# Kernel optimization log

Measured on AMD Instinct MI355X. Metric: run time of the kernel, lower is better.

The kernel has to match this reference:

```python
import jax, jax.numpy as jnp
import numpy as np

NUM_TABLES = 10
EMB_DIM = 3
VOCAB = 1_000_000
N_IDX = 4_000_000
N_BAGS = 100_000


def setup_inputs() -> dict:
    key = jax.random.key(0)
    k_idx, k_off, k_w = jax.random.split(key, 3)
    eb_input = jax.random.randint(k_idx, (N_IDX,), 0, VOCAB, dtype=jnp.int64)
    # EmbeddingBag offsets: sorted, first element must be 0, values in [0, N_IDX)
    eb_offset = jnp.sort(jax.random.randint(k_off, (N_BAGS,), 0, N_IDX, dtype=jnp.int64))
    eb_offset = eb_offset.at[0].set(0)
    # torch.nn.EmbeddingBag default init: N(0, 1)
    W = jax.random.normal(k_w, (NUM_TABLES, VOCAB, EMB_DIM), dtype=jnp.float32)
    return {"eb_input": eb_input, "eb_offset": eb_offset, "W": W}


def _bag_sums(eb_input, eb_offset, W):
    # segment id for each index position: bag b covers [offset[b], offset[b+1])
    n = eb_input.shape[0]
    seg = jnp.searchsorted(eb_offset, jnp.arange(n), side="right") - 1  # [N]
    gathered = W[:, eb_input, :]  # [T, N, D] irregular gather
    # sum-pool per bag for every table
    per_bag = jax.vmap(lambda g: jax.ops.segment_sum(g, seg, num_segments=eb_offset.shape[0]))(gathered)  # [T, B, D]
    return per_bag


def reference(eb_input, eb_offset, W):
    per_bag = _bag_sums(eb_input, eb_offset, W)  # [10, B, 3]
    outs = [per_bag[i] for i in range(NUM_TABLES)]
    outs[5] = jnp.sum(outs[5], axis=1, keepdims=True)  # [B, 1]
    outs[6] = jnp.sum(outs[6], axis=1, keepdims=True)  # [B, 1]
    cat = jnp.concatenate(outs, axis=1)  # [B, 26]
    return jnp.sum(cat, axis=0)  # [26]
```

## Files before the change

### kernel.cpp

```cpp
#include <hip/hip_runtime.h>

#define VOCAB 1000000
#define NUM_TABLES 10
#define OUT_SIZE 26
#define BUCKET_BITS 12
#define BPB 4096
#define NBUCKETS 245
#define CHUNK 4096
#define MAXSRC 1024
#define GSTRIDE 256
#define NPB NBUCKETS
#define NSERIES 30


__global__ void __launch_bounds__(256) scatter_kernel(
    const int* __restrict__ idx, int n,
    unsigned short* __restrict__ scat,
    unsigned int* __restrict__ gs32)
{
    __shared__ unsigned int lcount[256];
    __shared__ unsigned int sc[256];
    __shared__ __align__(16) unsigned short stage[CHUNK];
    const int tid = threadIdx.x;
    lcount[tid] = 0u;
    __syncthreads();

    const int4* idx4 = (const int4*)idx;
    const int n4 = n >> 2;
    const int base4 = blockIdx.x * (CHUNK / 4);
    int4 q[4];
    bool val[4];
    unsigned rank[16];
    unsigned bkt[16];
#pragma unroll
    for (int j = 0; j < 4; ++j) {
        int i4 = base4 + j * 256 + tid;
        val[j] = (i4 < n4);
        if (val[j]) q[j] = idx4[i4];
    }
#pragma unroll
    for (int j = 0; j < 4; ++j) {
        if (val[j]) {
            unsigned v[4] = {(unsigned)q[j].x, (unsigned)q[j].y, (unsigned)q[j].z, (unsigned)q[j].w};
#pragma unroll
            for (int e = 0; e < 4; ++e) {
                bkt[j * 4 + e] = v[e] >> BUCKET_BITS;
                rank[j * 4 + e] = atomicAdd(&lcount[bkt[j * 4 + e]], 1u);
            }
        }
    }
    unsigned trank[3], tbkt[3];
    int tcnt = 0;
    if (blockIdx.x == gridDim.x - 1 && tid == 0) {
        for (int i = n4 * 4; i < n; ++i) {
            unsigned u = (unsigned)idx[i];
            tbkt[tcnt] = u >> BUCKET_BITS;
            trank[tcnt] = atomicAdd(&lcount[tbkt[tcnt]], 1u);
            ++tcnt;
        }
    }
    __syncthreads();
    unsigned cnt = (tid < NBUCKETS) ? lcount[tid] : 0u;
    sc[tid] = cnt;
    __syncthreads();
#pragma unroll
    for (int off = 1; off < 256; off <<= 1) {
        unsigned v = sc[tid];
        unsigned a = (tid >= off) ? sc[tid - off] : 0u;
        __syncthreads();
        sc[tid] = v + a;
        __syncthreads();
    }
    unsigned excl = sc[tid] - cnt;
    if (tid < NBUCKETS) gs32[(size_t)blockIdx.x * GSTRIDE + tid] = excl | (cnt << 16);
    lcount[tid] = excl;
    __syncthreads();
#pragma unroll
    for (int j = 0; j < 4; ++j) {
        if (val[j]) {
            unsigned v[4] = {(unsigned)q[j].x, (unsigned)q[j].y, (unsigned)q[j].z, (unsigned)q[j].w};
#pragma unroll
            for (int e = 0; e < 4; ++e) {
                unsigned k = j * 4 + e;
                stage[lcount[bkt[k]] + rank[k]] = (unsigned short)(v[e] & (BPB - 1));
            }
        }
    }
    if (blockIdx.x == gridDim.x - 1 && tid == 0) {
        for (int i = 0; i < tcnt; ++i) {
            unsigned u = (unsigned)idx[n4 * 4 + i];
            stage[lcount[tbkt[i]] + trank[i]] = (unsigned short)(u & (BPB - 1));
        }
    }
    __syncthreads();
    uint4* dst = (uint4*)(scat + (size_t)blockIdx.x * CHUNK);
    const uint4* src = (const uint4*)stage;
#pragma unroll
    for (int j = 0; j < 2; ++j) dst[j * 256 + tid] = src[j * 256 + tid];
}

__device__ inline float wave_reduce(float v) {
#pragma unroll
    for (int o = 32; o > 0; o >>= 1) v += __shfl_down(v, o, 64);
    return v;
}

__global__ void __launch_bounds__(1024) bucket_reduce_kernel(
    const unsigned short* __restrict__ scat,
    const unsigned int* __restrict__ gs32, int nsrc,
    const float* __restrict__ W,
    float* __restrict__ partials)
{
    __shared__ __align__(16) unsigned int h[BPB];
    __shared__ float sm[16][NSERIES];
    const int b = blockIdx.x;
    const int tid = threadIdx.x;
    for (int i = tid; i < BPB; i += 1024) h[i] = 0u;
    __syncthreads();
    if (tid < nsrc) {
        unsigned g32 = gs32[(size_t)tid * GSTRIDE + b];
        unsigned s = g32 & 0xffffu, c = g32 >> 16;
        const unsigned short* p = scat + (size_t)tid * CHUNK + s;
        unsigned k = 0;
        for (; k + 4 <= c; k += 4) {
            unsigned short a0 = p[k], a1 = p[k + 1], a2 = p[k + 2], a3 = p[k + 3];
            atomicAdd(&h[a0], 1u);
            atomicAdd(&h[a1], 1u);
            atomicAdd(&h[a2], 1u);
            atomicAdd(&h[a3], 1u);
        }
        for (; k < c; ++k) atomicAdd(&h[p[k]], 1u);
    }
    __syncthreads();

    const int nbg = min(BPB, VOCAB - b * BPB) >> 2;
    float acc[NUM_TABLES][3];
#pragma unroll
    for (int t = 0; t < NUM_TABLES; ++t) {
        acc[t][0] = 0.f; acc[t][1] = 0.f; acc[t][2] = 0.f;
    }
    if (tid < nbg) {
        uint4 c4 = ((const uint4*)h)[tid];
        float c0 = (float)c4.x, c1 = (float)c4.y, c2 = (float)c4.z, c3 = (float)c4.w;
        const int g = b * (BPB / 4) + tid;
#pragma unroll
        for (int t = 0; t < NUM_TABLES; ++t) {
            const float4* __restrict__ W4 = (const float4*)(W + (size_t)t * VOCAB * 3);
            float4 w0 = W4[3 * g + 0];
            float4 w1 = W4[3 * g + 1];
            float4 w2 = W4[3 * g + 2];
            acc[t][0] += c0 * w0.x + c1 * w0.w + c2 * w1.z + c3 * w2.y;
            acc[t][1] += c0 * w0.y + c1 * w1.x + c2 * w1.w + c3 * w2.z;
            acc[t][2] += c0 * w0.z + c1 * w1.y + c2 * w2.x + c3 * w2.w;
        }
    }
    const int wave = tid >> 6, lane = tid & 63;
#pragma unroll
    for (int t = 0; t < NUM_TABLES; ++t) {
#pragma unroll
        for (int d = 0; d < 3; ++d) {
            float v = wave_reduce(acc[t][d]);
            if (lane == 0) sm[wave][t * 3 + d] = v;
        }
    }
    __syncthreads();
    if (tid < NSERIES) {
        float v = 0.f;
#pragma unroll
        for (int w = 0; w < 16; ++w) v += sm[w][tid];
        partials[(size_t)tid * NPB + b] = v;
    }
}

__global__ void __launch_bounds__(1024) final_kernel(const float* __restrict__ partials,
                                                     float* __restrict__ out) {
    __shared__ float ts[32];
    const int tid = threadIdx.x;
    const int srs = tid >> 5;
    const int j = tid & 31;
    float v = 0.f;
    if (srs < NSERIES) {
        const float* p = partials + (size_t)srs * NPB;
#pragma unroll
        for (int k = 0; k < 8; ++k) {
            int i = k * 32 + j;
            if (i < NPB) v += p[i];
        }
    }
#pragma unroll
    for (int off = 16; off > 0; off >>= 1) v += __shfl_down(v, off);
    if (j == 0 && srs < NSERIES) ts[srs] = v;
    __syncthreads();
    if (tid < OUT_SIZE) {
        float r;
        if (tid < 15) r = ts[tid];
        else if (tid == 15) r = ts[15] + ts[16] + ts[17];
        else if (tid == 16) r = ts[18] + ts[19] + ts[20];
        else r = ts[tid + 4];
        out[tid] = r;
    }
}


__global__ void zero_kernel_fb(unsigned int* __restrict__ hist, float* __restrict__ out) {
    int i = blockIdx.x * blockDim.x + threadIdx.x;
    int n4 = VOCAB / 4;
    if (i < n4) ((uint4*)hist)[i] = make_uint4(0u, 0u, 0u, 0u);
    if (i < OUT_SIZE) out[i] = 0.0f;
}

__global__ void hist_kernel_fb(const int* __restrict__ idx, unsigned int* __restrict__ hist, int n) {
    int i = blockIdx.x * blockDim.x + threadIdx.x;
    int i4 = i * 4;
    if (i4 + 3 < n) {
        int4 v = ((const int4*)idx)[i];
        atomicAdd(&hist[v.x], 1u);
        atomicAdd(&hist[v.y], 1u);
        atomicAdd(&hist[v.z], 1u);
        atomicAdd(&hist[v.w], 1u);
    } else {
        for (int j = i4; j < n; ++j) atomicAdd(&hist[idx[j]], 1u);
    }
}

#define RTHREADS 256

__global__ void __launch_bounds__(RTHREADS) reduce_kernel_fb(const float* __restrict__ W,
                                                             const unsigned int* __restrict__ hist,
                                                             float* __restrict__ out) {
    const int t = blockIdx.x / 64;
    const int b = blockIdx.x % 64;
    const float4* __restrict__ W4 = (const float4*)(W + (size_t)t * VOCAB * 3);
    const uint4* __restrict__ h4 = (const uint4*)hist;
    const int ngroups = VOCAB / 4;
    float a0 = 0.f, a1 = 0.f, a2 = 0.f;
    const int stride = 64 * RTHREADS;
    for (int g = b * RTHREADS + (int)threadIdx.x; g < ngroups; g += stride) {
        uint4 c4 = h4[g];
        float4 w0 = W4[3 * g + 0];
        float4 w1 = W4[3 * g + 1];
        float4 w2 = W4[3 * g + 2];
        float c0 = (float)c4.x, c1 = (float)c4.y, c2 = (float)c4.z, c3 = (float)c4.w;
        a0 += c0 * w0.x + c1 * w0.w + c2 * w1.z + c3 * w2.y;
        a1 += c0 * w0.y + c1 * w1.x + c2 * w1.w + c3 * w2.z;
        a2 += c0 * w0.z + c1 * w1.y + c2 * w2.x + c3 * w2.w;
    }
    a0 = wave_reduce(a0);
    a1 = wave_reduce(a1);
    a2 = wave_reduce(a2);
    __shared__ float s[3][4];
    int wave = threadIdx.x >> 6;
    int lane = threadIdx.x & 63;
    if (lane == 0) { s[0][wave] = a0; s[1][wave] = a1; s[2][wave] = a2; }
    __syncthreads();
    if (threadIdx.x == 0) {
        float r0 = s[0][0] + s[0][1] + s[0][2] + s[0][3];
        float r1 = s[1][0] + s[1][1] + s[1][2] + s[1][3];
        float r2 = s[2][0] + s[2][1] + s[2][2] + s[2][3];
        if (t == 5) atomicAdd(&out[15], r0 + r1 + r2);
        else if (t == 6) atomicAdd(&out[16], r0 + r1 + r2);
        else {
            int base = (t < 5) ? t * 3 : 17 + (t - 7) * 3;
            atomicAdd(&out[base + 0], r0);
            atomicAdd(&out[base + 1], r1);
            atomicAdd(&out[base + 2], r2);
        }
    }
}


extern "C" void kernel_launch(void* const* d_in, const int* in_sizes, int n_in,
                              void* d_out, int out_size, void* d_ws, size_t ws_size,
                              hipStream_t stream) {
    const int* eb_input = (const int*)d_in[0];
    const float* W = (const float*)d_in[2];
    float* out = (float*)d_out;
    int n_idx = in_sizes[0];

    const int nsrc = (n_idx + CHUNK - 1) / CHUNK;
    const size_t scat_bytes = (size_t)MAXSRC * CHUNK * 2;
    const size_t gs_off = scat_bytes;
    const size_t gs_bytes = (size_t)MAXSRC * GSTRIDE * 4;
    const size_t part_off = (gs_off + gs_bytes + 255) & ~(size_t)255;
    const size_t need = part_off + (size_t)NSERIES * NPB * 4;

    if (nsrc <= MAXSRC && ws_size >= need) {
        unsigned short* scat = (unsigned short*)d_ws;
        unsigned int* gs32 = (unsigned int*)((char*)d_ws + gs_off);
        float* partials = (float*)((char*)d_ws + part_off);

        scatter_kernel<<<nsrc, 256, 0, stream>>>(eb_input, n_idx, scat, gs32);
        bucket_reduce_kernel<<<NBUCKETS, 1024, 0, stream>>>(scat, gs32, nsrc, W, partials);
        final_kernel<<<1, 1024, 0, stream>>>(partials, out);
    } else {
        unsigned int* hist = (unsigned int*)d_ws;
        int zblocks = (VOCAB / 4 + 255) / 256;
        zero_kernel_fb<<<zblocks, 256, 0, stream>>>(hist, out);
        int hthreads = (n_idx + 3) / 4;
        int hblocks = (hthreads + 255) / 256;
        hist_kernel_fb<<<hblocks, 256, 0, stream>>>(eb_input, hist, n_idx);
        reduce_kernel_fb<<<NUM_TABLES * 64, RTHREADS, 0, stream>>>(W, hist, out);
    }
}
```

Measured before the change: 214.7 us.

## Split bucket reduction across table pairs to raise block-level parallelism

The bucket reduction kernel now launches five blocks per bucket, each handling two of the ten tables with 512 threads, instead of one 1024-thread block per bucket covering all tables. This raises the grid from 245 to 1225 blocks to fill the GPU better and spreads the weight-table reads. In exchange, each bucket's histogram is rebuilt five times, multiplying the scatter-read and LDS atomic work.

Result: slower. 221.4 us (+3.1%).

```diff
diff --git a/kernel.cpp b/kernel.cpp
--- a/kernel.cpp
+++ b/kernel.cpp
@@ -11,6 +11,8 @@
 #define GSTRIDE 256
 #define NPB NBUCKETS
 #define NSERIES 30
+#define TSPLIT 5
+#define PTHREADS 512
 
 
 __global__ void __launch_bounds__(256) scatter_kernel(
@@ -105,22 +107,25 @@
     return v;
 }
 
-__global__ void __launch_bounds__(1024) bucket_reduce_kernel(
+__global__ void __launch_bounds__(PTHREADS) bucket_pair_kernel(
     const unsigned short* __restrict__ scat,
     const unsigned int* __restrict__ gs32, int nsrc,
     const float* __restrict__ W,
     float* __restrict__ partials)
 {
     __shared__ __align__(16) unsigned int h[BPB];
-    __shared__ float sm[16][NSERIES];
-    const int b = blockIdx.x;
+    __shared__ float sm[8][6];
+    const int b = blockIdx.x / TSPLIT;
+    const int tp = blockIdx.x % TSPLIT;
     const int tid = threadIdx.x;
-    for (int i = tid; i < BPB; i += 1024) h[i] = 0u;
-    __syncthreads();
-    if (tid < nsrc) {
-        unsigned g32 = gs32[(size_t)tid * GSTRIDE + b];
-        unsigned s = g32 & 0xffffu, c = g32 >> 16;
-        const unsigned short* p = scat + (size_t)tid * CHUNK + s;
+#pragma unroll
+    for (int i = 0; i < BPB / 4 / PTHREADS; ++i)
+        ((uint4*)h)[i * PTHREADS + tid] = make_uint4(0u, 0u, 0u, 0u);
+    __syncthreads();
+    for (int s = tid; s < nsrc; s += PTHREADS) {
+        unsigned g32 = gs32[(size_t)s * GSTRIDE + b];
+        unsigned st = g32 & 0xffffu, c = g32 >> 16;
+        const unsigned short* p = scat + (size_t)s * CHUNK + st;
         unsigned k = 0;
         for (; k + 4 <= c; k += 4) {
             unsigned short a0 = p[k], a1 = p[k + 1], a2 = p[k + 2], a3 = p[k + 3];
@@ -134,41 +139,45 @@
     __syncthreads();
 
     const int nbg = min(BPB, VOCAB - b * BPB) >> 2;
-    float acc[NUM_TABLES][3];
-#pragma unroll
-    for (int t = 0; t < NUM_TABLES; ++t) {
-        acc[t][0] = 0.f; acc[t][1] = 0.f; acc[t][2] = 0.f;
-    }
-    if (tid < nbg) {
-        uint4 c4 = ((const uint4*)h)[tid];
-        float c0 = (float)c4.x, c1 = (float)c4.y, c2 = (float)c4.z, c3 = (float)c4.w;
-        const int g = b * (BPB / 4) + tid;
-#pragma unroll
-        for (int t = 0; t < NUM_TABLES; ++t) {
-            const float4* __restrict__ W4 = (const float4*)(W + (size_t)t * VOCAB * 3);
-            float4 w0 = W4[3 * g + 0];
-            float4 w1 = W4[3 * g + 1];
-            float4 w2 = W4[3 * g + 2];
-            acc[t][0] += c0 * w0.x + c1 * w0.w + c2 * w1.z + c3 * w2.y;
-            acc[t][1] += c0 * w0.y + c1 * w1.x + c2 * w1.w + c3 * w2.z;
-            acc[t][2] += c0 * w0.z + c1 * w1.y + c2 * w2.x + c3 * w2.w;
+    float acc[2][3];
+#pragma unroll
+    for (int i = 0; i < 2; ++i) { acc[i][0] = 0.f; acc[i][1] = 0.f; acc[i][2] = 0.f; }
+#pragma unroll
+    for (int rep = 0; rep < 2; ++rep) {
+        const int gg = rep * PTHREADS + tid;
+        if (gg < nbg) {
+            uint4 c4 = ((const uint4*)h)[gg];
+            float c0 = (float)c4.x, c1 = (float)c4.y, c2 = (float)c4.z, c3 = (float)c4.w;
+            const int g = b * (BPB / 4) + gg;
+#pragma unroll
+            for (int i = 0; i < 2; ++i) {
+                const int t = tp * 2 + i;
+                const float4* __restrict__ W4 = (const float4*)(W + (size_t)t * VOCAB * 3);
+                float4 w0 = W4[3 * g + 0];
+                float4 w1 = W4[3 * g + 1];
+                float4 w2 = W4[3 * g + 2];
+                acc[i][0] += c0 * w0.x + c1 * w0.w + c2 * w1.z + c3 * w2.y;
+                acc[i][1] += c0 * w0.y + c1 * w1.x + c2 * w1.w + c3 * w2.z;
+                acc[i][2] += c0 * w0.z + c1 * w1.y + c2 * w2.x + c3 * w2.w;
+            }
         }
     }
     const int wave = tid >> 6, lane = tid & 63;
 #pragma unroll
-    for (int t = 0; t < NUM_TABLES; ++t) {
+    for (int i = 0; i < 2; ++i) {
 #pragma unroll
         for (int d = 0; d < 3; ++d) {
-            float v = wave_reduce(acc[t][d]);
-            if (lane == 0) sm[wave][t * 3 + d] = v;
-        }
-    }
-    __syncthreads();
-    if (tid < NSERIES) {
+            float v = wave_reduce(acc[i][d]);
+            if (lane == 0) sm[wave][i * 3 + d] = v;
+        }
+    }
+    __syncthreads();
+    if (tid < 6) {
         float v = 0.f;
 #pragma unroll
-        for (int w = 0; w < 16; ++w) v += sm[w][tid];
-        partials[(size_t)tid * NPB + b] = v;
+        for (int w = 0; w < 8; ++w) v += sm[w][tid];
+        const int srs = (tp * 2 + tid / 3) * 3 + (tid % 3);
+        partials[(size_t)srs * NPB + b] = v;
     }
 }
 
@@ -290,7 +299,7 @@
         float* partials = (float*)((char*)d_ws + part_off);
 
         scatter_kernel<<<nsrc, 256, 0, stream>>>(eb_input, n_idx, scat, gs32);
-        bucket_reduce_kernel<<<NBUCKETS, 1024, 0, stream>>>(scat, gs32, nsrc, W, partials);
+        bucket_pair_kernel<<<NBUCKETS * TSPLIT, PTHREADS, 0, stream>>>(scat, gs32, nsrc, W, partials);
         final_kernel<<<1, 1024, 0, stream>>>(partials, out);
     } else {
         unsigned int* hist = (unsigned int*)d_ws;
```
